# Kernel optimization log

Measured on AMD Instinct MI355X. Metric: run time of the kernel, lower is better.

Reference implementation:

```python
import jax, jax.numpy as jnp
import numpy as np

N = 20000      # num_nodes
H = 150        # hidden_channels
R = 35         # num_relations
B = 5          # num_blocks  -> block dims 30x30
E = 640000     # num_edges
IB = H // B


def _xavier(key, shape):
    fan_in, fan_out = shape[-2], shape[-1]
    lim = jnp.sqrt(6.0 / (fan_in + fan_out))
    return jax.random.uniform(key, shape, jnp.float32, -lim, lim)


def setup_inputs() -> dict:
    key = jax.random.key(0)
    ks = jax.random.split(key, 10)
    edge_index = jax.random.randint(ks[0], (2, E), 0, N, dtype=jnp.int64)
    edge_type = jax.random.randint(ks[1], (E,), 0, R, dtype=jnp.int64)
    return {
        "node_emb": _xavier(ks[2], (N, H)),
        "w1": _xavier(ks[3], (R, B, IB, IB)),      # relation block-diagonal weights
        "root1": _xavier(ks[4], (H, H)),
        "b1": jnp.zeros((H,), jnp.float32),
        "w2": _xavier(ks[5], (R, B, IB, IB)),
        "root2": _xavier(ks[6], (H, H)),
        "b2": jnp.zeros((H,), jnp.float32),
        "edge_index": edge_index,
        "edge_type": edge_type,
    }


def _rgcn_layer(x, w, root, bias, src, dst, etype):
    # PyG RGCNConv with num_blocks: per-relation block-diag transform of source
    # features, mean-aggregated per (dst, relation), summed over relations,
    # plus dense root transform and bias.
    # Linearity lets us aggregate (mean) FIRST, then transform: cheaper + exact.
    seg = dst * R + etype                                   # [E] segment per (node, rel)
    xs = x[src]                                             # [E, H] gather
    sums = jax.ops.segment_sum(xs, seg, num_segments=N * R)  # [N*R, H]
    cnt = jax.ops.segment_sum(jnp.ones((src.shape[0],), x.dtype), seg,
                              num_segments=N * R)           # [N*R]
    mean = sums / jnp.maximum(cnt, 1.0)[:, None]            # zero where no edges
    a = mean.reshape(N, R, B, IB)
    agg = jnp.einsum('nrbi,rbio->nbo', a, w).reshape(N, H)  # sum over relations
    return agg + x @ root + bias


def reference(node_emb, w1, root1, b1, w2, root2, b2, edge_index, edge_type):
    src, dst = edge_index[0], edge_index[1]
    x = _rgcn_layer(node_emb, w1, root1, b1, src, dst, edge_type)
    x = jax.nn.relu(x)
    # dropout p=0.2 is a no-op in eval mode
    x = _rgcn_layer(x, w2, root2, b2, src, dst, edge_type)
    return x
```

## Files before the change

kernel.cpp:

```cpp
#include <hip/hip_runtime.h>
#include <hip/hip_fp16.h>

#define H 150
#define RNUM 35
#define BNUM 5
#define IB 30

typedef unsigned short ushort_t;
typedef unsigned int uint_t;
using bf16x8 = __attribute__((ext_vector_type(8))) short;
using f32x4  = __attribute__((ext_vector_type(4))) float;

__device__ __forceinline__ ushort_t f2bf(float x) {
    union { float f; unsigned u; } v; v.f = x;
    unsigned u = v.u;
    return (ushort_t)((u + 0x7FFF + ((u >> 16) & 1)) >> 16);
}
__device__ __forceinline__ float bfLo(uint_t u) {
    union { unsigned u; float f; } v; v.u = u << 16; return v.f;
}
__device__ __forceinline__ float bfHi(uint_t u) {
    union { unsigned u; float f; } v; v.u = u & 0xffff0000u; return v.f;
}


__global__ void k_count(const int* __restrict__ ei, const int* __restrict__ et,
                        int E_, int* __restrict__ cnt) {
    for (int e = blockIdx.x * blockDim.x + threadIdx.x; e < E_; e += gridDim.x * blockDim.x) {
        int d = ei[E_ + e];
        int r = et[e];
        atomicAdd(&cnt[d * RNUM + r], 1);
    }
}

#define SPT 2
#define SCAN_BLOCK 256
#define SCAN_SPAN (SPT * SCAN_BLOCK)

__global__ void k_scanA(const int* __restrict__ cnt, int N_,
                        int* __restrict__ blkN, int* __restrict__ blkD) {
    __shared__ int sn[SCAN_BLOCK], sd[SCAN_BLOCK];
    int t = threadIdx.x;
    int base = blockIdx.x * SCAN_SPAN + t * SPT;
    int tn = 0, td = 0;
    for (int k = 0; k < SPT; ++k) {
        int d = base + k;
        if (d < N_) {
            for (int r = 0; r < RNUM; ++r) {
                int c = cnt[d * RNUM + r];
                if (c) { tn++; td += c; }
            }
        }
    }
    sn[t] = tn; sd[t] = td;
    __syncthreads();
    if (t == 0) {
        int an = 0, ad = 0;
        for (int i = 0; i < SCAN_BLOCK; ++i) { an += sn[i]; ad += sd[i]; }
        blkN[blockIdx.x] = an; blkD[blockIdx.x] = ad;
    }
}

__global__ void k_scanB(const int* __restrict__ blkN, const int* __restrict__ blkD,
                        int* __restrict__ blkBN, int* __restrict__ blkBD, int nblk) {
    if (threadIdx.x == 0 && blockIdx.x == 0) {
        int an = 0, ad = 0;
        for (int i = 0; i < nblk; ++i) {
            blkBN[i] = an; blkBD[i] = ad;
            an += blkN[i]; ad += blkD[i];
        }
    }
}

__global__ void k_scanC(const int* __restrict__ cnt, int N_,
                        const int* __restrict__ blkBN, const int* __restrict__ blkBD,
                        int* __restrict__ dstbase, int* __restrict__ segoff,
                        int* __restrict__ segidx, int* __restrict__ relhist2) {
    __shared__ int sn[SCAN_BLOCK], sd[SCAN_BLOCK];
    __shared__ int lhist[RNUM];
    int t = threadIdx.x;
    for (int i = t; i < RNUM; i += SCAN_BLOCK) lhist[i] = 0;
    int base = blockIdx.x * SCAN_SPAN + t * SPT;
    int tn = 0, td = 0;
    for (int k = 0; k < SPT; ++k) {
        int d = base + k;
        if (d < N_) {
            for (int r = 0; r < RNUM; ++r) {
                int c = cnt[d * RNUM + r];
                if (c) { tn++; td += c; }
            }
        }
    }
    sn[t] = tn; sd[t] = td;
    __syncthreads();
    if (t == 0) {
        int an = blkBN[blockIdx.x], ad = blkBD[blockIdx.x];
        for (int i = 0; i < SCAN_BLOCK; ++i) {
            int a = sn[i], b = sd[i];
            sn[i] = an; sd[i] = ad;
            an += a; ad += b;
        }
    }
    __syncthreads();
    int sb = sn[t], eb = sd[t];
    for (int k = 0; k < SPT; ++k) {
        int d = base + k;
        if (d < N_) {
            dstbase[d] = sb;
            for (int r = 0; r < RNUM; ++r) {
                int cell = d * RNUM + r;
                int c = cnt[cell];
                segoff[cell] = eb;
                if (c) { segidx[cell] = sb; sb++; eb += c; atomicAdd(&lhist[r], 1); }
            }
            if (d == N_ - 1) dstbase[N_] = sb;
        }
    }
    __syncthreads();
    for (int i = t; i < RNUM; i += SCAN_BLOCK)
        if (lhist[i]) atomicAdd(&relhist2[i], lhist[i]);
}

__global__ void k_relbase(const int* __restrict__ relhist2, int* __restrict__ relbase2,
                          int* __restrict__ tprefix) {
    if (threadIdx.x == 0 && blockIdx.x == 0) {
        int a = 0, tp = 0;
        for (int r = 0; r < RNUM; ++r) {
            relbase2[r] = a; tprefix[r] = tp;
            a += relhist2[r];
            tp += (relhist2[r] + 15) >> 4;
        }
        relbase2[RNUM] = a; tprefix[RNUM] = tp;
    }
}

__global__ void k_scatter2(const int* __restrict__ ei, const int* __restrict__ et,
                           int E_, int* __restrict__ segoff, int* __restrict__ ssrc2) {
    int e = blockIdx.x * blockDim.x + threadIdx.x;
    if (e >= E_) return;
    int r = et[e];
    int d = ei[E_ + e];
    int pos = atomicAdd(&segoff[d * RNUM + r], 1);
    ssrc2[pos] = ei[e];
}

__global__ void k_relassign(const int* __restrict__ cnt, const int* __restrict__ segoff,
                            const int* __restrict__ segidx, int Ncells,
                            const int* __restrict__ relbase2, int* __restrict__ relfill2,
                            int4* __restrict__ rec) {
    __shared__ int lh[RNUM];
    __shared__ int lbase[RNUM];
    for (int i = threadIdx.x; i < RNUM; i += blockDim.x) lh[i] = 0;
    __syncthreads();
    const int stride = gridDim.x * blockDim.x;
    for (int cell = blockIdx.x * blockDim.x + threadIdx.x; cell < Ncells; cell += stride)
        if (cnt[cell]) atomicAdd(&lh[cell % RNUM], 1);
    __syncthreads();
    for (int i = threadIdx.x; i < RNUM; i += blockDim.x) {
        int c = lh[i];
        lbase[i] = relbase2[i] + (c ? atomicAdd(&relfill2[i], c) : 0);
        lh[i] = 0;
    }
    __syncthreads();
    for (int cell = blockIdx.x * blockDim.x + threadIdx.x; cell < Ncells; cell += stride) {
        int c = cnt[cell];
        if (c) {
            int r = cell % RNUM;
            int pos = lbase[r] + atomicAdd(&lh[r], 1);
            rec[pos] = make_int4(segidx[cell], segoff[cell] - c, c, 0);
        }
    }
}

__global__ void k_prep(const float* __restrict__ w1, const float* __restrict__ w2,
                       ushort_t* __restrict__ wb1, ushort_t* __restrict__ wb2,
                       const float* __restrict__ r1, const float* __restrict__ r2,
                       ushort_t* __restrict__ B1, ushort_t* __restrict__ B2,
                       const float* __restrict__ x, ushort_t* __restrict__ xbf, int N_) {
    const int tot = RNUM * BNUM * 2 * 16 * 32;
    const int t2 = 2 * tot;
    const int t3 = t2 + 2 * 160 * 160;
    const long long t4 = (long long)t3 + (long long)N_ * 160;
    long long i = (long long)blockIdx.x * blockDim.x + threadIdx.x;
    if (i < t2) {
        int idx = (int)i;
        const float* w = (idx < tot) ? w1 : w2;
        ushort_t* wb = (idx < tot) ? wb1 : wb2;
        int q = (idx < tot) ? idx : idx - tot;
        int kj = q & 7;
        int kg = (q >> 3) & 3;
        int cl = (q >> 5) & 15;
        int nh = (q >> 9) & 1;
        int rb = q >> 10;
        int k = kg * 8 + kj;
        int col = nh * 16 + cl;
        ushort_t v = 0;
        if (k < IB && col < IB) v = f2bf(w[(rb * IB + k) * IB + col]);
        wb[q] = v;
    } else if (i < t3) {
        int k = (int)(i - t2);
        const float* src = (k < 160 * 160) ? r1 : r2;
        ushort_t* dst = (k < 160 * 160) ? B1 : B2;
        if (k >= 160 * 160) k -= 160 * 160;
        int row = k / 160, col = k - row * 160;
        dst[k] = (row < H && col < H) ? f2bf(src[row * H + col]) : 0;
    } else if (i < t4) {
        long long k = i - t3;
        int n = (int)(k / 160), c = (int)(k - (long long)n * 160);
        xbf[k] = (c < H) ? f2bf(x[(size_t)n * H + c]) : 0;
    }
}

__global__ __launch_bounds__(256) void k_rootmm(const ushort_t* __restrict__ Abf,
                                                const ushort_t* __restrict__ Bbf,
                                                const float* __restrict__ bias,
                                                float* __restrict__ Cout, int N_) {
    int nt = blockIdx.y;
    int wv = threadIdx.x >> 6, l = threadIdx.x & 63;
    int lr = l & 15, lk = l >> 4;
    bf16x8 bfr[5];
    #pragma unroll
    for (int ks = 0; ks < 5; ++ks) {
        #pragma unroll
        for (int j = 0; j < 8; ++j)
            bfr[ks][j] = (short)Bbf[(ks * 32 + lk * 8 + j) * 160 + nt * 16 + lr];
    }
    int mtiles = N_ / 16;
    int col = nt * 16 + lr;
    float bv = (col < H) ? bias[col] : 0.f;
    for (int mt = blockIdx.x * 4 + wv; mt < mtiles; mt += gridDim.x * 4) {
        f32x4 acc = {0.f, 0.f, 0.f, 0.f};
        const ushort_t* arow = Abf + (size_t)(mt * 16 + lr) * 160 + lk * 8;
        #pragma unroll
        for (int ks = 0; ks < 5; ++ks) {
            bf16x8 af = *reinterpret_cast<const bf16x8*>(arow + ks * 32);
            acc = __builtin_amdgcn_mfma_f32_16x16x32_bf16(af, bfr[ks], acc, 0, 0, 0);
        }
        if (col < H) {
            #pragma unroll
            for (int reg = 0; reg < 4; ++reg)
                Cout[(size_t)(mt * 16 + lk * 4 + reg) * H + col] = acc[reg] + bv;
        }
    }
}


#define ASTRIDE 168

__global__ __launch_bounds__(256, 4)
void k_seg(const int4* __restrict__ rec, const int* __restrict__ relbase2,
           const int* __restrict__ tprefix,
           const int* __restrict__ ssrc2, const ushort_t* __restrict__ wbf,
           const ushort_t* __restrict__ xbf, __half* __restrict__ tseg,
           const int* __restrict__ rowLoP, const int* __restrict__ rowHiP) {
    __shared__ ushort_t Abuf[4][16 * ASTRIDE];
    __shared__ int relb[RNUM + 1], tpre[RNUM + 1];
    int t = threadIdx.x, wv = t >> 6, l = t & 63;
    int lr = l & 15, kg = l >> 4;
    if (t < RNUM + 1) { relb[t] = relbase2[t]; tpre[t] = tprefix[t]; }

    {
        uint_t* az = reinterpret_cast<uint_t*>(&Abuf[wv][0]);
        for (int i = l; i < 16 * ASTRIDE / 2; i += 64) az[i] = 0;
    }
    __syncthreads();
    int rowLo = rowLoP[0], rowHi = rowHiP[0];
    int ntile_tot = tpre[RNUM];

    int i0 = 2 * l;
    int uA = ((i0 / 30) * 32 + (i0 % 30)) >> 1;
    int i1 = 128 + 2 * l;
    int uB = ((i1 / 30) * 32 + (i1 % 30)) >> 1;

    for (int ti = blockIdx.x * 4 + wv; ti < ntile_tot; ti += gridDim.x * 4) {
        int r_lo = 0, r_hi = RNUM;
        while (r_hi - r_lo > 1) {
            int m = (r_lo + r_hi) >> 1;
            if (tpre[m] <= ti) r_lo = m; else r_hi = m;
        }
        int r = r_lo;
        int base = relb[r];
        int nseg = relb[r + 1] - base;
        int sbeg = (ti - tpre[r]) << 4;

        bf16x8 bfr[BNUM][2];
        #pragma unroll
        for (int b = 0; b < BNUM; ++b)
            #pragma unroll
            for (int nh = 0; nh < 2; ++nh)
                bfr[b][nh] = *reinterpret_cast<const bf16x8*>(
                    wbf + ((size_t)((r * BNUM + b) * 2 + nh) * 512) + lr * 32 + kg * 8);

        int4 myrec = make_int4(0x7fffffff, 0, 1, 0);
        if (l < 16 && sbeg + l < nseg) myrec = rec[base + sbeg + l];

        uint_t* Au = reinterpret_cast<uint_t*>(&Abuf[wv][0]);
        for (int s = 0; s < 16; ++s) {
            int row = __builtin_amdgcn_readfirstlane(__shfl(myrec.x, s));
            if (row < rowLo || row >= rowHi) continue;
            int eo = __builtin_amdgcn_readfirstlane(__shfl(myrec.y, s));
            int c  = __builtin_amdgcn_readfirstlane(__shfl(myrec.z, s));
            int src0 = ssrc2[eo];
            const uint_t* rowU = reinterpret_cast<const uint_t*>(xbf + (size_t)src0 * 160);
            uint_t u0 = rowU[l];
            uint_t u1 = 0;
            if (l < 11) u1 = rowU[64 + l];
            if (c == 1) {
                Au[s * 84 + uA] = u0;
                if (l < 11) Au[s * 84 + uB] = u1;
            } else {
                float a0 = bfLo(u0), a1 = bfHi(u0);
                float a2 = bfLo(u1), a3 = bfHi(u1);
                for (int k = 1; k < c; ++k) {
                    int src = ssrc2[eo + k];
                    const uint_t* rU = reinterpret_cast<const uint_t*>(
                        xbf + (size_t)src * 160);
                    uint_t v0 = rU[l];
                    a0 += bfLo(v0); a1 += bfHi(v0);
                    if (l < 11) {
                        uint_t v1 = rU[64 + l];
                        a2 += bfLo(v1); a3 += bfHi(v1);
                    }
                }
                float inv = 1.0f / (float)c;
                Au[s * 84 + uA] = (uint_t)f2bf(a0 * inv) | ((uint_t)f2bf(a1 * inv) << 16);
                if (l < 11)
                    Au[s * 84 + uB] = (uint_t)f2bf(a2 * inv) | ((uint_t)f2bf(a3 * inv) << 16);
            }
        }

        int rg[4]; bool rok[4];
        #pragma unroll
        for (int q = 0; q < 4; ++q) {
            rg[q] = __shfl(myrec.x, kg * 4 + q);
            rok[q] = (rg[q] >= rowLo) && (rg[q] < rowHi);
        }

        #pragma unroll
        for (int b = 0; b < BNUM; ++b) {
            bf16x8 af = *reinterpret_cast<const bf16x8*>(
                &Abuf[wv][lr * ASTRIDE + b * 32 + kg * 8]);
            f32x4 z = {0.f, 0.f, 0.f, 0.f};
            f32x4 acc0 = __builtin_amdgcn_mfma_f32_16x16x32_bf16(af, bfr[b][0], z, 0, 0, 0);
            f32x4 acc1 = __builtin_amdgcn_mfma_f32_16x16x32_bf16(af, bfr[b][1], z, 0, 0, 0);
            #pragma unroll
            for (int q = 0; q < 4; ++q) {
                if (rok[q]) {
                    __half* orow = tseg + (size_t)(rg[q] - rowLo) * H + b * IB;
                    orow[lr] = __float2half(acc0[q]);
                    if (lr < 14) orow[16 + lr] = __float2half(acc1[q]);
                }
            }
        }
    }
}


__global__ __launch_bounds__(256)
void k_aggadd(const __half* __restrict__ tseg, const int* __restrict__ dstbase,
              const float* __restrict__ rootsrc, float* __restrict__ fout,
              ushort_t* __restrict__ Abf, int relu, int s0, int s1) {
    int t = threadIdx.x, wv = t >> 6, l = t & 63;
    int segBase = dstbase[s0];
    for (int d = s0 + blockIdx.x * 4 + wv; d < s1; d += gridDim.x * 4) {
        int a = dstbase[d], bnd = dstbase[d + 1];
        const float* brow = rootsrc + (size_t)d * H;
        float2 acc0 = *reinterpret_cast<const float2*>(brow + 2 * l);
        float2 acc1 = make_float2(0.f, 0.f);
        if (l < 11) acc1 = *reinterpret_cast<const float2*>(brow + 128 + 2 * l);
        for (int s = a; s < bnd; ++s) {
            const __half2* trow = reinterpret_cast<const __half2*>(
                tseg + (size_t)(s - segBase) * H);
            float2 v = __half22float2(trow[l]);
            acc0.x += v.x; acc0.y += v.y;
            if (l < 11) {
                float2 v1 = __half22float2(trow[64 + l]);
                acc1.x += v1.x; acc1.y += v1.y;
            }
        }
        if (relu) {
            acc0.x = fmaxf(acc0.x, 0.f); acc0.y = fmaxf(acc0.y, 0.f);
            acc1.x = fmaxf(acc1.x, 0.f); acc1.y = fmaxf(acc1.y, 0.f);
        }
        if (fout) {
            float* frow = fout + (size_t)d * H;
            *reinterpret_cast<float2*>(frow + 2 * l) = acc0;
            if (l < 11) *reinterpret_cast<float2*>(frow + 128 + 2 * l) = acc1;
        }
        if (Abf) {
            ushort_t* arow = Abf + (size_t)d * 160;
            uint_t p0 = (uint_t)f2bf(acc0.x) | ((uint_t)f2bf(acc0.y) << 16);
            *reinterpret_cast<uint_t*>(arow + 2 * l) = p0;
            if (l < 11) {
                uint_t p1 = (uint_t)f2bf(acc1.x) | ((uint_t)f2bf(acc1.y) << 16);
                *reinterpret_cast<uint_t*>(arow + 128 + 2 * l) = p1;
            }
            if (l < 5) *reinterpret_cast<uint_t*>(arow + 150 + 2 * l) = 0;
        }
    }
}

extern "C" void kernel_launch(void* const* d_in, const int* in_sizes, int n_in,
                              void* d_out, int out_size, void* d_ws, size_t ws_size,
                              hipStream_t stream) {
    const float* node_emb = (const float*)d_in[0];
    const float* w1 = (const float*)d_in[1];
    const float* root1 = (const float*)d_in[2];
    const float* b1 = (const float*)d_in[3];
    const float* w2 = (const float*)d_in[4];
    const float* root2 = (const float*)d_in[5];
    const float* b2 = (const float*)d_in[6];
    const int* edge_index = (const int*)d_in[7];
    const int* edge_type = (const int*)d_in[8];
    int N_ = in_sizes[0] / H;
    int E_ = in_sizes[8];
    float* out = (float*)d_out;

    const int Ncells = N_ * RNUM;
    const int wbtot = RNUM * BNUM * 2 * 16 * 32;

    int* ws = (int*)d_ws;
    size_t off = 0;
    int* cnt      = ws + off; off += Ncells;
    int* relhist2 = ws + off; off += 64;
    int* relfill2 = ws + off; off += 64;
    size_t zero_units = off;
    int* relbase2 = ws + off; off += 64;
    int* tprefix  = ws + off; off += 64;
    int* blkN     = ws + off; off += 64;
    int* blkD     = ws + off; off += 64;
    int* blkBN    = ws + off; off += 64;
    int* blkBD    = ws + off; off += 64;
    int* dstbase  = ws + off; off += N_ + 2;
    int* segoff   = ws + off; off += Ncells;
    int* segidx   = ws + off; off += Ncells;
    int* ssrc2    = ws + off; off += E_;
    off = (off + 3) & ~(size_t)3;
    int4* rec     = (int4*)(ws + off); off += (size_t)4 * Ncells;
    ushort_t* wbf1 = (ushort_t*)(ws + off); off += wbtot / 2;
    ushort_t* wbf2 = (ushort_t*)(ws + off); off += wbtot / 2;
    ushort_t* Bbf1 = (ushort_t*)(ws + off); off += 12800;
    ushort_t* Bbf2 = (ushort_t*)(ws + off); off += 12800;
    ushort_t* xbf  = (ushort_t*)(ws + off); off += (size_t)N_ * 160 / 2;
    ushort_t* Abf  = (ushort_t*)(ws + off); off += (size_t)N_ * 160 / 2;
    float* rootbuf = (float*)(ws + off); off += (size_t)N_ * H;
    __half* tseg  = (__half*)(ws + off);
    size_t tsegOffB = off * 4;

    size_t availB = (ws_size > tsegOffB) ? (ws_size - tsegOffB) : 0;
    long long dps_ll = (long long)(availB / ((size_t)RNUM * H * 2));
    int dps = (dps_ll > N_) ? N_ : (int)dps_ll;
    if (dps < 1) dps = 1;
    int nstripe = (N_ + dps - 1) / dps;

    hipMemsetAsync(cnt, 0, zero_units * 4, stream);

    k_count<<<512, 256, 0, stream>>>(edge_index, edge_type, E_, cnt);
    int nscan = (N_ + SCAN_SPAN - 1) / SCAN_SPAN;
    k_scanA<<<nscan, SCAN_BLOCK, 0, stream>>>(cnt, N_, blkN, blkD);
    k_scanB<<<1, 64, 0, stream>>>(blkN, blkD, blkBN, blkBD, nscan);
    k_scanC<<<nscan, SCAN_BLOCK, 0, stream>>>(cnt, N_, blkBN, blkBD, dstbase, segoff,
                                              segidx, relhist2);
    k_relbase<<<1, 64, 0, stream>>>(relhist2, relbase2, tprefix);
    k_scatter2<<<(E_ + 255) / 256, 256, 0, stream>>>(edge_index, edge_type, E_, segoff, ssrc2);
    k_relassign<<<64, 256, 0, stream>>>(cnt, segoff, segidx, Ncells, relbase2, relfill2, rec);
    long long preptot = 2LL * wbtot + 2 * 160 * 160 + (long long)N_ * 160;
    k_prep<<<(int)((preptot + 255) / 256), 256, 0, stream>>>(
        w1, w2, wbf1, wbf2, root1, root2, Bbf1, Bbf2, node_emb, xbf, N_);

    const int SEG_GRID = 1792;

    k_rootmm<<<dim3(40, 10), 256, 0, stream>>>(xbf, Bbf1, b1, rootbuf, N_);
    for (int st = 0; st < nstripe; ++st) {
        int s0 = st * dps;
        int s1 = s0 + dps; if (s1 > N_) s1 = N_;
        k_seg<<<SEG_GRID, 256, 0, stream>>>(rec, relbase2, tprefix, ssrc2, wbf1, xbf, tseg,
                                            dstbase + s0, dstbase + s1);
        k_aggadd<<<1280, 256, 0, stream>>>(tseg, dstbase, rootbuf, (float*)nullptr, Abf,
                                           1, s0, s1);
    }

    k_rootmm<<<dim3(40, 10), 256, 0, stream>>>(Abf, Bbf2, b2, out, N_);
    for (int st = 0; st < nstripe; ++st) {
        int s0 = st * dps;
        int s1 = s0 + dps; if (s1 > N_) s1 = N_;
        k_seg<<<SEG_GRID, 256, 0, stream>>>(rec, relbase2, tprefix, ssrc2, wbf2, Abf, tseg,
                                            dstbase + s0, dstbase + s1);
        k_aggadd<<<1280, 256, 0, stream>>>(tseg, dstbase, out, out, (ushort_t*)nullptr,
                                           0, s0, s1);
    }
}
```

Before: 443.0 us.

## Fold relation bucketing into scan kernels and drop relassign and relbase passes

Per-block relation histograms are now computed in the first scan pass. The single-block middle scan turns them into per-block relation bases and the global relbase/tprefix arrays. The final scan pass writes the per-relation segment records directly, which removes two kernel launches, the segidx array and a full extra pass over the cell counts. In exchange, the middle scan kernel does more serial work, and the order of records within a relation now depends on shared-memory atomics instead of the old relassign ordering.

```diff
diff --git a/kernel.cpp b/kernel.cpp
--- a/kernel.cpp
+++ b/kernel.cpp
@@ -38,9 +38,13 @@
 #define SCAN_SPAN (SPT * SCAN_BLOCK)
 
 __global__ void k_scanA(const int* __restrict__ cnt, int N_,
-                        int* __restrict__ blkN, int* __restrict__ blkD) {
+                        int* __restrict__ blkN, int* __restrict__ blkD,
+                        int* __restrict__ blkRelH) {
     __shared__ int sn[SCAN_BLOCK], sd[SCAN_BLOCK];
+    __shared__ int lhist[RNUM];
     int t = threadIdx.x;
+    for (int i = t; i < RNUM; i += SCAN_BLOCK) lhist[i] = 0;
+    __syncthreads();
     int base = blockIdx.x * SCAN_SPAN + t * SPT;
     int tn = 0, td = 0;
     for (int k = 0; k < SPT; ++k) {
@@ -48,7 +52,7 @@
         if (d < N_) {
             for (int r = 0; r < RNUM; ++r) {
                 int c = cnt[d * RNUM + r];
-                if (c) { tn++; td += c; }
+                if (c) { tn++; td += c; atomicAdd(&lhist[r], 1); }
             }
         }
     }
@@ -59,27 +63,62 @@
         for (int i = 0; i < SCAN_BLOCK; ++i) { an += sn[i]; ad += sd[i]; }
         blkN[blockIdx.x] = an; blkD[blockIdx.x] = ad;
     }
+    for (int i = t; i < RNUM; i += SCAN_BLOCK)
+        blkRelH[blockIdx.x * RNUM + i] = lhist[i];
 }
 
 __global__ void k_scanB(const int* __restrict__ blkN, const int* __restrict__ blkD,
-                        int* __restrict__ blkBN, int* __restrict__ blkBD, int nblk) {
-    if (threadIdx.x == 0 && blockIdx.x == 0) {
+                        const int* __restrict__ blkRelH, int nblk,
+                        int* __restrict__ blkBN, int* __restrict__ blkBD,
+                        int* __restrict__ blkRelBase, int* __restrict__ relbase2,
+                        int* __restrict__ tprefix) {
+    __shared__ int relTot[RNUM];
+    __shared__ int relB[RNUM];
+    int t = threadIdx.x;
+    if (t == 0) {
         int an = 0, ad = 0;
         for (int i = 0; i < nblk; ++i) {
             blkBN[i] = an; blkBD[i] = ad;
             an += blkN[i]; ad += blkD[i];
         }
     }
+    if (t < RNUM) {
+        int s = 0;
+        for (int b = 0; b < nblk; ++b) s += blkRelH[b * RNUM + t];
+        relTot[t] = s;
+    }
+    __syncthreads();
+    if (t == 0) {
+        int a = 0, tp = 0;
+        for (int r = 0; r < RNUM; ++r) {
+            relbase2[r] = a; relB[r] = a; tprefix[r] = tp;
+            a += relTot[r];
+            tp += (relTot[r] + 15) >> 4;
+        }
+        relbase2[RNUM] = a; tprefix[RNUM] = tp;
+    }
+    __syncthreads();
+    if (t < RNUM) {
+        int run = relB[t];
+        for (int b = 0; b < nblk; ++b) {
+            blkRelBase[b * RNUM + t] = run;
+            run += blkRelH[b * RNUM + t];
+        }
+    }
 }
 
 __global__ void k_scanC(const int* __restrict__ cnt, int N_,
                         const int* __restrict__ blkBN, const int* __restrict__ blkBD,
+                        const int* __restrict__ blkRelBase,
                         int* __restrict__ dstbase, int* __restrict__ segoff,
-                        int* __restrict__ segidx, int* __restrict__ relhist2) {
+                        int4* __restrict__ rec) {
     __shared__ int sn[SCAN_BLOCK], sd[SCAN_BLOCK];
-    __shared__ int lhist[RNUM];
+    __shared__ int lrank[RNUM], lbase[RNUM];
     int t = threadIdx.x;
-    for (int i = t; i < RNUM; i += SCAN_BLOCK) lhist[i] = 0;
+    for (int i = t; i < RNUM; i += SCAN_BLOCK) {
+        lrank[i] = 0;
+        lbase[i] = blkRelBase[blockIdx.x * RNUM + i];
+    }
     int base = blockIdx.x * SCAN_SPAN + t * SPT;
     int tn = 0, td = 0;
     for (int k = 0; k < SPT; ++k) {
@@ -111,26 +150,14 @@
                 int cell = d * RNUM + r;
                 int c = cnt[cell];
                 segoff[cell] = eb;
-                if (c) { segidx[cell] = sb; sb++; eb += c; atomicAdd(&lhist[r], 1); }
+                if (c) {
+                    int pos = lbase[r] + atomicAdd(&lrank[r], 1);
+                    rec[pos] = make_int4(sb, eb, c, 0);
+                    sb++; eb += c;
+                }
             }
             if (d == N_ - 1) dstbase[N_] = sb;
         }
-    }
-    __syncthreads();
-    for (int i = t; i < RNUM; i += SCAN_BLOCK)
-        if (lhist[i]) atomicAdd(&relhist2[i], lhist[i]);
-}
-
-__global__ void k_relbase(const int* __restrict__ relhist2, int* __restrict__ relbase2,
-                          int* __restrict__ tprefix) {
-    if (threadIdx.x == 0 && blockIdx.x == 0) {
-        int a = 0, tp = 0;
-        for (int r = 0; r < RNUM; ++r) {
-            relbase2[r] = a; tprefix[r] = tp;
-            a += relhist2[r];
-            tp += (relhist2[r] + 15) >> 4;
-        }
-        relbase2[RNUM] = a; tprefix[RNUM] = tp;
     }
 }
 
@@ -142,34 +169,6 @@
     int d = ei[E_ + e];
     int pos = atomicAdd(&segoff[d * RNUM + r], 1);
     ssrc2[pos] = ei[e];
-}
-
-__global__ void k_relassign(const int* __restrict__ cnt, const int* __restrict__ segoff,
-                            const int* __restrict__ segidx, int Ncells,
-                            const int* __restrict__ relbase2, int* __restrict__ relfill2,
-                            int4* __restrict__ rec) {
-    __shared__ int lh[RNUM];
-    __shared__ int lbase[RNUM];
-    for (int i = threadIdx.x; i < RNUM; i += blockDim.x) lh[i] = 0;
-    __syncthreads();
-    const int stride = gridDim.x * blockDim.x;
-    for (int cell = blockIdx.x * blockDim.x + threadIdx.x; cell < Ncells; cell += stride)
-        if (cnt[cell]) atomicAdd(&lh[cell % RNUM], 1);
-    __syncthreads();
-    for (int i = threadIdx.x; i < RNUM; i += blockDim.x) {
-        int c = lh[i];
-        lbase[i] = relbase2[i] + (c ? atomicAdd(&relfill2[i], c) : 0);
-        lh[i] = 0;
-    }
-    __syncthreads();
-    for (int cell = blockIdx.x * blockDim.x + threadIdx.x; cell < Ncells; cell += stride) {
-        int c = cnt[cell];
-        if (c) {
-            int r = cell % RNUM;
-            int pos = lbase[r] + atomicAdd(&lh[r], 1);
-            rec[pos] = make_int4(segidx[cell], segoff[cell] - c, c, 0);
-        }
-    }
 }
 
 __global__ void k_prep(const float* __restrict__ w1, const float* __restrict__ w2,
@@ -422,8 +421,6 @@
     int* ws = (int*)d_ws;
     size_t off = 0;
     int* cnt      = ws + off; off += Ncells;
-    int* relhist2 = ws + off; off += 64;
-    int* relfill2 = ws + off; off += 64;
     size_t zero_units = off;
     int* relbase2 = ws + off; off += 64;
     int* tprefix  = ws + off; off += 64;
@@ -431,9 +428,10 @@
     int* blkD     = ws + off; off += 64;
     int* blkBN    = ws + off; off += 64;
     int* blkBD    = ws + off; off += 64;
+    int* blkRelH  = ws + off; off += 64 * RNUM;
+    int* blkRelB  = ws + off; off += 64 * RNUM;
     int* dstbase  = ws + off; off += N_ + 2;
     int* segoff   = ws + off; off += Ncells;
-    int* segidx   = ws + off; off += Ncells;
     int* ssrc2    = ws + off; off += E_;
     off = (off + 3) & ~(size_t)3;
     int4* rec     = (int4*)(ws + off); off += (size_t)4 * Ncells;
@@ -457,13 +455,12 @@
 
     k_count<<<512, 256, 0, stream>>>(edge_index, edge_type, E_, cnt);
     int nscan = (N_ + SCAN_SPAN - 1) / SCAN_SPAN;
-    k_scanA<<<nscan, SCAN_BLOCK, 0, stream>>>(cnt, N_, blkN, blkD);
-    k_scanB<<<1, 64, 0, stream>>>(blkN, blkD, blkBN, blkBD, nscan);
-    k_scanC<<<nscan, SCAN_BLOCK, 0, stream>>>(cnt, N_, blkBN, blkBD, dstbase, segoff,
-                                              segidx, relhist2);
-    k_relbase<<<1, 64, 0, stream>>>(relhist2, relbase2, tprefix);
+    k_scanA<<<nscan, SCAN_BLOCK, 0, stream>>>(cnt, N_, blkN, blkD, blkRelH);
+    k_scanB<<<1, 64, 0, stream>>>(blkN, blkD, blkRelH, nscan, blkBN, blkBD,
+                                  blkRelB, relbase2, tprefix);
+    k_scanC<<<nscan, SCAN_BLOCK, 0, stream>>>(cnt, N_, blkBN, blkBD, blkRelB,
+                                              dstbase, segoff, rec);
     k_scatter2<<<(E_ + 255) / 256, 256, 0, stream>>>(edge_index, edge_type, E_, segoff, ssrc2);
-    k_relassign<<<64, 256, 0, stream>>>(cnt, segoff, segidx, Ncells, relbase2, relfill2, rec);
     long long preptot = 2LL * wbtot + 2 * 160 * 160 + (long long)N_ * 160;
     k_prep<<<(int)((preptot + 255) / 256), 256, 0, stream>>>(
         w1, w2, wbf1, wbf2, root1, root2, Bbf1, Bbf2, node_emb, xbf, N_);
```

Result: faster. 420.9 us (-5.0%).
